# Optimization experiments

Hardware: AMD Instinct MI355X
Metric: run time of the kernel (lower is better)

The kernel has to match this reference:

```python
import jax, jax.numpy as jnp
import numpy as np

B, N, G, T, D = 32, 512, 64, 16, 256
E, M = 500000, 1024
NEG = jnp.float32(-1e10)


def setup_inputs() -> dict:
    key = jax.random.key(0)
    ks = jax.random.split(key, 8)
    scope_token_reprs = jax.random.normal(ks[0], (B, N, T, D), dtype=jnp.float32)
    goal_token_reprs = jax.random.normal(ks[1], (B, G, T, D), dtype=jnp.float32)
    W = jax.random.normal(ks[2], (1, D, D), dtype=jnp.float32) / np.sqrt(D)
    bias = jax.random.normal(ks[3], (1,), dtype=jnp.float32)
    src = jax.random.randint(ks[4], (E,), 0, B * N)
    tgt = jax.random.randint(ks[5], (E,), 0, B * G)
    edge_index = jnp.stack([src, tgt], axis=0)
    lm_mask_idx = jax.random.randint(ks[6], (M,), 0, B * N * T)
    batch_pts = lm_mask_idx // (N * T)  # consistent: each masked token belongs to its own batch element
    tree_mask = jax.random.uniform(ks[7], (B, N)) < 0.7
    return {
        'scope_token_reprs': scope_token_reprs,
        'goal_token_reprs': goal_token_reprs,
        'W': W,
        'bias': bias,
        'edge_index': edge_index,
        'lm_mask_idx': lm_mask_idx,
        'batch_pts': batch_pts,
        'tree_mask': tree_mask,
    }


def reference(scope_token_reprs, goal_token_reprs, W, bias, edge_index, lm_mask_idx, batch_pts, tree_mask):
    dim = scope_token_reprs.shape[-1]
    # --- predict_lemmas: edge gather + bilinear scoring ---
    scope_type = scope_token_reprs[:, :, 0].reshape(-1, dim)  # [B*N, D]
    goal_type = goal_token_reprs[:, :, 0].reshape(-1, dim)    # [B*G, D]
    sources = scope_type[edge_index[0]]                        # [E, D]
    targets = goal_type[edge_index[1]]                         # [E, D]
    lemma_preds = jnp.einsum('ed,df,ef->e', sources, W[0], targets) + bias[0]  # [E]
    # --- predict_masks: masked-token dot against candidate type reprs ---
    mask_reprs = scope_token_reprs.reshape(-1, dim)[lm_mask_idx]  # [M, D]
    type_reprs = scope_token_reprs[:, :, 0]                        # [B, N, D]
    candidates = type_reprs[batch_pts]                             # [M, N, D]
    candidate_mask = tree_mask[batch_pts]                          # [M, N]
    lm_preds = jnp.einsum('md,mnd->mn', mask_reprs, candidates)    # [M, N]
    lm_preds = jnp.where(candidate_mask, lm_preds, NEG)
    return lemma_preds, lm_preds
```

## Files before the change

kernel.cpp:

```cpp
#include <hip/hip_runtime.h>

#define B_   32
#define N_   512
#define G_   64
#define T_   16
#define D_   256
#define E_   500000
#define M_   1024
#define S_   (B_ * N_)
#define TT_  2048
#define TD_  (T_ * D_)
#define NEG_ (-10000000000.0f)

#define WS_WT    0
#define WS_WGB   262144
#define WS_SCB   2097152
#define WS_FLAG  10485760

typedef short  short8 __attribute__((ext_vector_type(8)));

__device__ __forceinline__ unsigned short f2bf(float x) {
  union { float f; unsigned int u; } v; v.f = x;
  const unsigned int r = (v.u + 0x7fffu + ((v.u >> 16) & 1u)) >> 16;
  return (unsigned short)r;
}

__device__ __forceinline__ float bf2f(unsigned short u) {
  union { unsigned int u; float f; } v;
  v.u = ((unsigned int)u) << 16;
  return v.f;
}

__global__ __launch_bounds__(256) void detect_mask_dtype(
    const unsigned char* __restrict__ tm, int* __restrict__ flag) {
  __shared__ int sA, sB;
  if (threadIdx.x == 0) { sA = 0; sB = 0; }
  __syncthreads();
  int a = 0, b3 = 0;
  for (int i = threadIdx.x; i < B_ * N_; i += 256) {
    const int r = i & 3;
    const unsigned char v = tm[i];
    if (r == 1) a |= v;
    else if (r == 3) b3 |= v;
  }
  if (a)  atomicOr(&sA, 1);
  if (b3) atomicOr(&sB, 1);
  __syncthreads();
  if (threadIdx.x == 0) flag[0] = sA ? 1 : (sB ? 2 : 0);
}

__global__ __launch_bounds__(256) void transpose_w(
    const float* __restrict__ W, float* __restrict__ Wt) {
  __shared__ float tile[32][33];
  const int bi = blockIdx.x >> 3;
  const int bj = blockIdx.x & 7;
  const int tx = threadIdx.x & 31;
  const int ty = threadIdx.x >> 5;
#pragma unroll
  for (int r = 0; r < 4; r++)
    tile[ty + r * 8][tx] = W[(size_t)(bi * 32 + ty + r * 8) * D_ + bj * 32 + tx];
  __syncthreads();
#pragma unroll
  for (int r = 0; r < 4; r++)
    Wt[(size_t)(bj * 32 + ty + r * 8) * D_ + bi * 32 + tx] =
        tile[tx][ty + r * 8];
}

__global__ __launch_bounds__(256) void wg_gemm(
    const float* __restrict__ goal, const float* __restrict__ Wt,
    unsigned short* __restrict__ Wgb) {
  __shared__ float g[8][256];
  const int j0 = blockIdx.x * 8;
  const int d  = threadIdx.x;
  {
    const int lane = threadIdx.x & 63;
    const int r0   = threadIdx.x >> 6;
#pragma unroll
    for (int rr = 0; rr < 2; rr++) {
      const int row = rr * 4 + r0;
      const float4 v = *reinterpret_cast<const float4*>(
          goal + (size_t)(j0 + row) * TD_ + lane * 4);
      float* dst = &g[row][lane * 4];
      dst[0] = v.x; dst[1] = v.y; dst[2] = v.z; dst[3] = v.w;
    }
  }
  __syncthreads();
  float acc[8];
#pragma unroll
  for (int jj = 0; jj < 8; jj++) acc[jj] = 0.f;
#pragma unroll 4
  for (int f = 0; f < D_; f++) {
    const float w = Wt[(size_t)f * D_ + d];
#pragma unroll
    for (int jj = 0; jj < 8; jj++) acc[jj] = fmaf(g[jj][f], w, acc[jj]);
  }
#pragma unroll
  for (int jj = 0; jj < 8; jj++)
    Wgb[(size_t)(j0 + jj) * D_ + d] = f2bf(acc[jj]);
}

__global__ __launch_bounds__(256) void cast_scope(
    const float* __restrict__ scope, unsigned short* __restrict__ scb) {
  const int q   = blockIdx.x * 256 + threadIdx.x;
  const int row = q >> 6;
  const int c4  = q & 63;
  const float4 v =
      *reinterpret_cast<const float4*>(scope + (size_t)row * TD_ + c4 * 4);
  ushort4 o;
  o.x = f2bf(v.x); o.y = f2bf(v.y); o.z = f2bf(v.z); o.w = f2bf(v.w);
  *reinterpret_cast<ushort4*>(&scb[(size_t)row * D_ + c4 * 4]) = o;
}

__global__ __launch_bounds__(256) void edge_dot(
    const unsigned short* __restrict__ scb,
    const unsigned short* __restrict__ wgb,
    const int* __restrict__ edges, const float* __restrict__ bias,
    float* __restrict__ out) {
  const int tid = threadIdx.x;
  const int grp = tid >> 4;
  const int l   = tid & 15;
  const int e   = blockIdx.x * 16 + grp;
  const int s = edges[e];
  const int t = edges[E_ + e];
  const short8 a0 = *reinterpret_cast<const short8*>(&scb[(size_t)s * D_ + l * 8]);
  const short8 a1 = *reinterpret_cast<const short8*>(&scb[(size_t)s * D_ + 128 + l * 8]);
  const short8 b0 = *reinterpret_cast<const short8*>(&wgb[(size_t)t * D_ + l * 8]);
  const short8 b1 = *reinterpret_cast<const short8*>(&wgb[(size_t)t * D_ + 128 + l * 8]);
  float acc = 0.f;
#pragma unroll
  for (int i = 0; i < 8; i++) {
    acc = fmaf(bf2f((unsigned short)a0[i]), bf2f((unsigned short)b0[i]), acc);
    acc = fmaf(bf2f((unsigned short)a1[i]), bf2f((unsigned short)b1[i]), acc);
  }
  acc += __shfl_xor(acc, 1);
  acc += __shfl_xor(acc, 2);
  acc += __shfl_xor(acc, 4);
  acc += __shfl_xor(acc, 8);
  if (l == 0) out[e] = acc + bias[0];
}

__global__ __launch_bounds__(256) void lm_kernel(
    const float* __restrict__ scope, const int* __restrict__ lm_idx,
    const int* __restrict__ batch_pts, const void* __restrict__ tree_mask,
    const int* __restrict__ flag_p, float* __restrict__ out) {
  __shared__ float cand[32][260];
  __shared__ unsigned char tmask[32];
  __shared__ int mlist[M_];
  __shared__ int mcnt;
  const int b  = blockIdx.x >> 4;
  const int n0 = (blockIdx.x & 15) * 32;
  const int t  = threadIdx.x;

  if (t == 0) mcnt = 0;
  {
    const int lane = t & 63;
    const int r0   = t >> 6;
#pragma unroll
    for (int rr = 0; rr < 8; rr++) {
      const int row = rr * 4 + r0;
      const float4 v = *reinterpret_cast<const float4*>(
          scope + (size_t)(b * N_ + n0 + row) * TD_ + lane * 4);
      float* dst = &cand[row][lane * 4];
      dst[0] = v.x; dst[1] = v.y; dst[2] = v.z; dst[3] = v.w;
    }
  }
  const int flag = flag_p[0];
  if (t < 32) {
    const int n = b * N_ + n0 + t;
    int v;
    if (flag == 1)      v = ((const unsigned char*)tree_mask)[n] != 0;
    else if (flag == 2) v = ((const float*)tree_mask)[n] != 0.0f;
    else                v = ((const int*)tree_mask)[n] != 0;
    tmask[t] = (unsigned char)v;
  }
  __syncthreads();

#pragma unroll
  for (int c = 0; c < M_ / 256; c++) {
    const int m = c * 256 + t;
    if (batch_pts[m] == b) {
      const int p = atomicAdd(&mcnt, 1);
      mlist[p] = m;
    }
  }
  __syncthreads();
  const int cnt = mcnt;

  const int nl = t >> 3;
  const int kg = t & 7;
  for (int k = 0; k < cnt; k++) {
    const int m = mlist[k];
    const float4* q =
        reinterpret_cast<const float4*>(scope + (size_t)lm_idx[m] * D_);
    float acc = 0.f;
#pragma unroll
    for (int i = 0; i < 8; i++) {
      const int f4 = kg * 8 + i;
      const float4 qv = q[f4];
      const float* cp = &cand[nl][f4 * 4];
      acc += qv.x * cp[0] + qv.y * cp[1] + qv.z * cp[2] + qv.w * cp[3];
    }
    acc += __shfl_xor(acc, 1);
    acc += __shfl_xor(acc, 2);
    acc += __shfl_xor(acc, 4);
    if (kg == 0)
      out[(size_t)m * N_ + (n0 + nl)] = tmask[nl] ? acc : NEG_;
  }
}

extern "C" void kernel_launch(void* const* d_in, const int* in_sizes, int n_in,
                              void* d_out, int out_size, void* d_ws,
                              size_t ws_size, hipStream_t stream) {
  const float* scope = (const float*)d_in[0];
  const float* goal  = (const float*)d_in[1];
  const float* W     = (const float*)d_in[2];
  const float* bias  = (const float*)d_in[3];
  const int*   edges = (const int*)d_in[4];
  const int*   lmidx = (const int*)d_in[5];
  const int*   bpts  = (const int*)d_in[6];
  const void*  tmask = d_in[7];

  float* out = (float*)d_out;
  char*  ws  = (char*)d_ws;
  float*          Wt   = (float*)(ws + WS_WT);
  unsigned short* Wgb  = (unsigned short*)(ws + WS_WGB);
  unsigned short* scb  = (unsigned short*)(ws + WS_SCB);
  int*            flag = (int*)(ws + WS_FLAG);

  detect_mask_dtype<<<1, 256, 0, stream>>>((const unsigned char*)tmask, flag);
  transpose_w<<<64, 256, 0, stream>>>(W, Wt);
  wg_gemm<<<TT_ / 8, 256, 0, stream>>>(goal, Wt, Wgb);
  cast_scope<<<(S_ * 64) / 256, 256, 0, stream>>>(scope, scb);
  edge_dot<<<E_ / 16, 256, 0, stream>>>(scb, Wgb, edges, bias, out);
  lm_kernel<<<B_ * 16, 256, 0, stream>>>(scope, lmidx, bpts, tmask, flag,
                                         out + E_);
}
```

Baseline: 466.0 us.

## Fuse mask-dtype detection, W transpose, scope cast and LM scoring into one launch

Merges four small kernels into a single launch whose block index chooses the job: LM scoring blocks (each now detects the tree-mask dtype locally), bf16 cast blocks for the scope rows, and W-transpose blocks. This removes three launches and the global flag round-trip, and lets the independent stages overlap. The edge-dot kernel now gives each edge 8 lanes with four 16-byte loads per operand instead of 16 lanes, which shortens the shuffle reduction. The cost is that every LM block re-reads the whole mask to decide the dtype, and the fused kernel's larger shared-memory footprint may lower occupancy for the cast blocks.

```diff
diff --git a/kernel.cpp b/kernel.cpp
--- a/kernel.cpp
+++ b/kernel.cpp
@@ -15,7 +15,6 @@
 #define WS_WT    0
 #define WS_WGB   262144
 #define WS_SCB   2097152
-#define WS_FLAG  10485760
 
 typedef short  short8 __attribute__((ext_vector_type(8)));
 
@@ -31,39 +30,135 @@
   return v.f;
 }
 
-__global__ __launch_bounds__(256) void detect_mask_dtype(
-    const unsigned char* __restrict__ tm, int* __restrict__ flag) {
-  __shared__ int sA, sB;
-  if (threadIdx.x == 0) { sA = 0; sB = 0; }
-  __syncthreads();
-  int a = 0, b3 = 0;
-  for (int i = threadIdx.x; i < B_ * N_; i += 256) {
-    const int r = i & 3;
-    const unsigned char v = tm[i];
-    if (r == 1) a |= v;
-    else if (r == 3) b3 |= v;
-  }
-  if (a)  atomicOr(&sA, 1);
-  if (b3) atomicOr(&sB, 1);
-  __syncthreads();
-  if (threadIdx.x == 0) flag[0] = sA ? 1 : (sB ? 2 : 0);
-}
-
-__global__ __launch_bounds__(256) void transpose_w(
-    const float* __restrict__ W, float* __restrict__ Wt) {
-  __shared__ float tile[32][33];
-  const int bi = blockIdx.x >> 3;
-  const int bj = blockIdx.x & 7;
-  const int tx = threadIdx.x & 31;
-  const int ty = threadIdx.x >> 5;
-#pragma unroll
-  for (int r = 0; r < 4; r++)
-    tile[ty + r * 8][tx] = W[(size_t)(bi * 32 + ty + r * 8) * D_ + bj * 32 + tx];
-  __syncthreads();
-#pragma unroll
-  for (int r = 0; r < 4; r++)
-    Wt[(size_t)(bj * 32 + ty + r * 8) * D_ + bi * 32 + tx] =
-        tile[tx][ty + r * 8];
+#define LM_BLOCKS   512
+#define CAST_BLOCKS 4096
+#define TW_BLOCKS   64
+#define SM_CAND     0
+#define SM_MLIST    33280
+#define SM_TMASK    37376
+#define SM_MCNT     37408
+#define SM_FA       37412
+#define SM_FB       37416
+#define SM_SIZE     37424
+
+__global__ __launch_bounds__(256) void fused_prep_lm(
+    const float* __restrict__ scope, const float* __restrict__ W,
+    float* __restrict__ Wt, unsigned short* __restrict__ scb,
+    const int* __restrict__ lm_idx, const int* __restrict__ batch_pts,
+    const void* __restrict__ tree_mask, float* __restrict__ out) {
+  __shared__ __align__(16) char smem[SM_SIZE];
+  const int bid = blockIdx.x;
+  const int t   = threadIdx.x;
+
+  if (bid < LM_BLOCKS) {
+    float (*cand)[260]   = reinterpret_cast<float(*)[260]>(smem + SM_CAND);
+    int*  mlist          = reinterpret_cast<int*>(smem + SM_MLIST);
+    unsigned char* tmask = reinterpret_cast<unsigned char*>(smem + SM_TMASK);
+    int*  mcnt           = reinterpret_cast<int*>(smem + SM_MCNT);
+    int*  fA             = reinterpret_cast<int*>(smem + SM_FA);
+    int*  fB             = reinterpret_cast<int*>(smem + SM_FB);
+    const int b  = bid >> 4;
+    const int n0 = (bid & 15) * 32;
+
+    if (t == 0) { *mcnt = 0; *fA = 0; *fB = 0; }
+    __syncthreads();
+
+    {
+      const uint4* tw = reinterpret_cast<const uint4*>(tree_mask);
+      unsigned int aa = 0, bb = 0;
+#pragma unroll
+      for (int i = 0; i < 4; i++) {
+        const uint4 w = tw[t + i * 256];
+        aa |= (w.x >> 8) & 0xffu;  bb |= w.x >> 24;
+        aa |= (w.y >> 8) & 0xffu;  bb |= w.y >> 24;
+        aa |= (w.z >> 8) & 0xffu;  bb |= w.z >> 24;
+        aa |= (w.w >> 8) & 0xffu;  bb |= w.w >> 24;
+      }
+      if (aa) atomicOr(fA, 1);
+      if (bb) atomicOr(fB, 1);
+    }
+
+    {
+      const int lane = t & 63;
+      const int r0   = t >> 6;
+#pragma unroll
+      for (int rr = 0; rr < 8; rr++) {
+        const int row = rr * 4 + r0;
+        const float4 v = *reinterpret_cast<const float4*>(
+            scope + (size_t)(b * N_ + n0 + row) * TD_ + lane * 4);
+        float* dst = &cand[row][lane * 4];
+        dst[0] = v.x; dst[1] = v.y; dst[2] = v.z; dst[3] = v.w;
+      }
+    }
+    __syncthreads();
+
+    const int flag = *fA ? 1 : (*fB ? 2 : 0);
+    if (t < 32) {
+      const int n = b * N_ + n0 + t;
+      int v;
+      if (flag == 1)      v = ((const unsigned char*)tree_mask)[n] != 0;
+      else if (flag == 2) v = ((const float*)tree_mask)[n] != 0.0f;
+      else                v = ((const int*)tree_mask)[n] != 0;
+      tmask[t] = (unsigned char)v;
+    }
+
+#pragma unroll
+    for (int c = 0; c < M_ / 256; c++) {
+      const int m = c * 256 + t;
+      if (batch_pts[m] == b) {
+        const int p = atomicAdd(mcnt, 1);
+        mlist[p] = m;
+      }
+    }
+    __syncthreads();
+    const int cnt = *mcnt;
+
+    const int nl = t >> 3;
+    const int kg = t & 7;
+    for (int k = 0; k < cnt; k++) {
+      const int m = mlist[k];
+      const float4* q =
+          reinterpret_cast<const float4*>(scope + (size_t)lm_idx[m] * D_);
+      float acc = 0.f;
+#pragma unroll
+      for (int i = 0; i < 8; i++) {
+        const int f4 = kg * 8 + i;
+        const float4 qv = q[f4];
+        const float* cp = &cand[nl][f4 * 4];
+        acc += qv.x * cp[0] + qv.y * cp[1] + qv.z * cp[2] + qv.w * cp[3];
+      }
+      acc += __shfl_xor(acc, 1);
+      acc += __shfl_xor(acc, 2);
+      acc += __shfl_xor(acc, 4);
+      if (kg == 0)
+        out[(size_t)m * N_ + (n0 + nl)] = tmask[nl] ? acc : NEG_;
+    }
+  } else if (bid < LM_BLOCKS + CAST_BLOCKS) {
+    const int q   = (bid - LM_BLOCKS) * 256 + t;
+    const int row = q >> 6;
+    const int c4  = q & 63;
+    const float4 v =
+        *reinterpret_cast<const float4*>(scope + (size_t)row * TD_ + c4 * 4);
+    ushort4 o;
+    o.x = f2bf(v.x); o.y = f2bf(v.y); o.z = f2bf(v.z); o.w = f2bf(v.w);
+    *reinterpret_cast<ushort4*>(&scb[(size_t)row * D_ + c4 * 4]) = o;
+  } else {
+    float (*tile)[33] = reinterpret_cast<float(*)[33]>(smem);
+    const int tb = bid - (LM_BLOCKS + CAST_BLOCKS);
+    const int bi = tb >> 3;
+    const int bj = tb & 7;
+    const int tx = t & 31;
+    const int ty = t >> 5;
+#pragma unroll
+    for (int r = 0; r < 4; r++)
+      tile[ty + r * 8][tx] =
+          W[(size_t)(bi * 32 + ty + r * 8) * D_ + bj * 32 + tx];
+    __syncthreads();
+#pragma unroll
+    for (int r = 0; r < 4; r++)
+      Wt[(size_t)(bj * 32 + ty + r * 8) * D_ + bi * 32 + tx] =
+          tile[tx][ty + r * 8];
+  }
 }
 
 __global__ __launch_bounds__(256) void wg_gemm(
@@ -99,113 +194,36 @@
     Wgb[(size_t)(j0 + jj) * D_ + d] = f2bf(acc[jj]);
 }
 
-__global__ __launch_bounds__(256) void cast_scope(
-    const float* __restrict__ scope, unsigned short* __restrict__ scb) {
-  const int q   = blockIdx.x * 256 + threadIdx.x;
-  const int row = q >> 6;
-  const int c4  = q & 63;
-  const float4 v =
-      *reinterpret_cast<const float4*>(scope + (size_t)row * TD_ + c4 * 4);
-  ushort4 o;
-  o.x = f2bf(v.x); o.y = f2bf(v.y); o.z = f2bf(v.z); o.w = f2bf(v.w);
-  *reinterpret_cast<ushort4*>(&scb[(size_t)row * D_ + c4 * 4]) = o;
-}
-
 __global__ __launch_bounds__(256) void edge_dot(
     const unsigned short* __restrict__ scb,
     const unsigned short* __restrict__ wgb,
     const int* __restrict__ edges, const float* __restrict__ bias,
     float* __restrict__ out) {
   const int tid = threadIdx.x;
-  const int grp = tid >> 4;
-  const int l   = tid & 15;
-  const int e   = blockIdx.x * 16 + grp;
+  const int grp = tid >> 3;
+  const int l   = tid & 7;
+  const int e   = blockIdx.x * 32 + grp;
   const int s = edges[e];
   const int t = edges[E_ + e];
-  const short8 a0 = *reinterpret_cast<const short8*>(&scb[(size_t)s * D_ + l * 8]);
-  const short8 a1 = *reinterpret_cast<const short8*>(&scb[(size_t)s * D_ + 128 + l * 8]);
-  const short8 b0 = *reinterpret_cast<const short8*>(&wgb[(size_t)t * D_ + l * 8]);
-  const short8 b1 = *reinterpret_cast<const short8*>(&wgb[(size_t)t * D_ + 128 + l * 8]);
+  const size_t sa = (size_t)s * D_;
+  const size_t ta = (size_t)t * D_;
+  short8 a[4], b[4];
+#pragma unroll
+  for (int i = 0; i < 4; i++) {
+    a[i] = *reinterpret_cast<const short8*>(&scb[sa + i * 64 + l * 8]);
+    b[i] = *reinterpret_cast<const short8*>(&wgb[ta + i * 64 + l * 8]);
+  }
   float acc = 0.f;
 #pragma unroll
-  for (int i = 0; i < 8; i++) {
-    acc = fmaf(bf2f((unsigned short)a0[i]), bf2f((unsigned short)b0[i]), acc);
-    acc = fmaf(bf2f((unsigned short)a1[i]), bf2f((unsigned short)b1[i]), acc);
-  }
+  for (int i = 0; i < 4; i++)
+#pragma unroll
+    for (int j = 0; j < 8; j++)
+      acc = fmaf(bf2f((unsigned short)a[i][j]),
+                 bf2f((unsigned short)b[i][j]), acc);
   acc += __shfl_xor(acc, 1);
   acc += __shfl_xor(acc, 2);
   acc += __shfl_xor(acc, 4);
-  acc += __shfl_xor(acc, 8);
   if (l == 0) out[e] = acc + bias[0];
-}
-
-__global__ __launch_bounds__(256) void lm_kernel(
-    const float* __restrict__ scope, const int* __restrict__ lm_idx,
-    const int* __restrict__ batch_pts, const void* __restrict__ tree_mask,
-    const int* __restrict__ flag_p, float* __restrict__ out) {
-  __shared__ float cand[32][260];
-  __shared__ unsigned char tmask[32];
-  __shared__ int mlist[M_];
-  __shared__ int mcnt;
-  const int b  = blockIdx.x >> 4;
-  const int n0 = (blockIdx.x & 15) * 32;
-  const int t  = threadIdx.x;
-
-  if (t == 0) mcnt = 0;
-  {
-    const int lane = t & 63;
-    const int r0   = t >> 6;
-#pragma unroll
-    for (int rr = 0; rr < 8; rr++) {
-      const int row = rr * 4 + r0;
-      const float4 v = *reinterpret_cast<const float4*>(
-          scope + (size_t)(b * N_ + n0 + row) * TD_ + lane * 4);
-      float* dst = &cand[row][lane * 4];
-      dst[0] = v.x; dst[1] = v.y; dst[2] = v.z; dst[3] = v.w;
-    }
-  }
-  const int flag = flag_p[0];
-  if (t < 32) {
-    const int n = b * N_ + n0 + t;
-    int v;
-    if (flag == 1)      v = ((const unsigned char*)tree_mask)[n] != 0;
-    else if (flag == 2) v = ((const float*)tree_mask)[n] != 0.0f;
-    else                v = ((const int*)tree_mask)[n] != 0;
-    tmask[t] = (unsigned char)v;
-  }
-  __syncthreads();
-
-#pragma unroll
-  for (int c = 0; c < M_ / 256; c++) {
-    const int m = c * 256 + t;
-    if (batch_pts[m] == b) {
-      const int p = atomicAdd(&mcnt, 1);
-      mlist[p] = m;
-    }
-  }
-  __syncthreads();
-  const int cnt = mcnt;
-
-  const int nl = t >> 3;
-  const int kg = t & 7;
-  for (int k = 0; k < cnt; k++) {
-    const int m = mlist[k];
-    const float4* q =
-        reinterpret_cast<const float4*>(scope + (size_t)lm_idx[m] * D_);
-    float acc = 0.f;
-#pragma unroll
-    for (int i = 0; i < 8; i++) {
-      const int f4 = kg * 8 + i;
-      const float4 qv = q[f4];
-      const float* cp = &cand[nl][f4 * 4];
-      acc += qv.x * cp[0] + qv.y * cp[1] + qv.z * cp[2] + qv.w * cp[3];
-    }
-    acc += __shfl_xor(acc, 1);
-    acc += __shfl_xor(acc, 2);
-    acc += __shfl_xor(acc, 4);
-    if (kg == 0)
-      out[(size_t)m * N_ + (n0 + nl)] = tmask[nl] ? acc : NEG_;
-  }
 }
 
 extern "C" void kernel_launch(void* const* d_in, const int* in_sizes, int n_in,
@@ -225,13 +243,9 @@
   float*          Wt   = (float*)(ws + WS_WT);
   unsigned short* Wgb  = (unsigned short*)(ws + WS_WGB);
   unsigned short* scb  = (unsigned short*)(ws + WS_SCB);
-  int*            flag = (int*)(ws + WS_FLAG);
-
-  detect_mask_dtype<<<1, 256, 0, stream>>>((const unsigned char*)tmask, flag);
-  transpose_w<<<64, 256, 0, stream>>>(W, Wt);
+
+  fused_prep_lm<<<LM_BLOCKS + CAST_BLOCKS + TW_BLOCKS, 256, 0, stream>>>(
+      scope, W, Wt, scb, lmidx, bpts, tmask, out + E_);
   wg_gemm<<<TT_ / 8, 256, 0, stream>>>(goal, Wt, Wgb);
-  cast_scope<<<(S_ * 64) / 256, 256, 0, stream>>>(scope, scb);
-  edge_dot<<<E_ / 16, 256, 0, stream>>>(scb, Wgb, edges, bias, out);
-  lm_kernel<<<B_ * 16, 256, 0, stream>>>(scope, lmidx, bpts, tmask, flag,
-                                         out + E_);
-}
+  edge_dot<<<E_ / 32, 256, 0, stream>>>(scb, Wgb, edges, bias, out);
+}
```

Measured after the change: 437.6 us. 6.1% less time.
